# Kernel tuning notes

Hardware: AMD Instinct MI355X
Metric: run time of the kernel (lower is better)

## Reference

```python
import jax, jax.numpy as jnp
import numpy as np

N_NODES = 50000
N_EDGES = 250000
D_IN, D_HID, D_OUT = 768, 256, 2


def _sage_conv(x, src, dst, W_l, b_l, W_r, n_nodes):
    # PyG SAGEConv (aggr='mean', root_weight=True):
    #   out[i] = lin_l(mean_{j in N(i)} x[j]) + lin_r(x[i])
    msg = x[src]  # [E, d] gather of source-node features
    agg = jax.ops.segment_sum(msg, dst, num_segments=n_nodes)
    cnt = jax.ops.segment_sum(jnp.ones((src.shape[0],), x.dtype), dst,
                              num_segments=n_nodes)
    agg = agg / jnp.maximum(cnt, 1.0)[:, None]
    return agg @ W_l.T + b_l + x @ W_r.T


def setup_inputs() -> dict:
    key = jax.random.key(0)
    ks = jax.random.split(key, 7)
    x = jax.random.normal(ks[0], (N_NODES, D_IN), dtype=jnp.float32)
    edge_index = jax.random.randint(ks[1], (2, N_EDGES), 0, N_NODES,
                                    dtype=jnp.int64)
    s1 = 1.0 / np.sqrt(D_IN)
    s2 = 1.0 / np.sqrt(D_HID)
    W1_l = jax.random.uniform(ks[2], (D_HID, D_IN), jnp.float32, -s1, s1)
    W1_r = jax.random.uniform(ks[3], (D_HID, D_IN), jnp.float32, -s1, s1)
    b1 = jnp.zeros((D_HID,), jnp.float32)
    W2_l = jax.random.uniform(ks[4], (D_OUT, D_HID), jnp.float32, -s2, s2)
    W2_r = jax.random.uniform(ks[5], (D_OUT, D_HID), jnp.float32, -s2, s2)
    b2 = jnp.zeros((D_OUT,), jnp.float32)
    return {"x": x, "edge_index": edge_index,
            "W1_l": W1_l, "b1": b1, "W1_r": W1_r,
            "W2_l": W2_l, "b2": b2, "W2_r": W2_r}


def reference(x, edge_index, W1_l, b1, W1_r, W2_l, b2, W2_r):
    src, dst = edge_index[0], edge_index[1]
    n = x.shape[0]
    h = _sage_conv(x, src, dst, W1_l, b1, W1_r, n)
    h = jax.nn.relu(h)
    # dropout is identity in eval mode (deterministic reference)
    out = _sage_conv(h, src, dst, W2_l, b2, W2_r, n)
    return out
```

## Files before the change

kernel.cpp:

```cpp
#include <hip/hip_runtime.h>
#include <stdint.h>


#define D_IN  768
#define D_HID 256
#define N1    512
#define KITERS (D_IN / 32)

typedef __attribute__((ext_vector_type(8))) short short8;
typedef __attribute__((ext_vector_type(4))) float f32x4;

__device__ __forceinline__ void async_copy16(const void* g, void* l) {
  __builtin_amdgcn_global_load_lds(
      (const __attribute__((address_space(1))) unsigned int*)g,
      (__attribute__((address_space(3))) unsigned int*)l,
      16, 0, 0);
}

__device__ __forceinline__ unsigned short f2bf(float f) {
  union { float f; unsigned u; } v; v.f = f;
  unsigned r = v.u + 0x7FFFu + ((v.u >> 16) & 1u);
  return (unsigned short)(r >> 16);
}

__device__ __forceinline__ float bf2f(unsigned short b) {
  union { unsigned u; float f; } v; v.u = ((unsigned)b) << 16;
  return v.f;
}


__global__ void cvtidx_k(const void* __restrict__ eidx,
                         int* __restrict__ src32, int* __restrict__ dst32,
                         int* __restrict__ counts, int E) {
  __shared__ int flag32;
  int tid = threadIdx.x;
  int i = blockIdx.x * 256 + tid;
  unsigned v = (i < E) ? ((const unsigned int*)eidx)[2 * (size_t)i + 1] : 0u;
  unsigned long long any = __ballot(v != 0u);
  if (tid == 0) flag32 = 0;
  __syncthreads();
  if ((tid & 63) == 0 && any) flag32 = 1;
  __syncthreads();
  if (i >= E) return;
  int s, d;
  if (flag32) {
    const int* p = (const int*)eidx;
    s = p[i]; d = p[E + i];
  } else {
    const long long* p = (const long long*)eidx;
    s = (int)p[i]; d = (int)p[E + i];
  }
  src32[i] = s;
  dst32[i] = d;
  atomicAdd(&counts[d], 1);
}

__global__ void scanA_k(const int* __restrict__ counts,
                        int* __restrict__ blockSums, int M) {
  __shared__ int ts[256];
  int b = blockIdx.x, t = threadIdx.x;
  int base = b * 1024 + t * 4;
  int s = 0;
#pragma unroll
  for (int k = 0; k < 4; k++) { int i = base + k; if (i < M) s += counts[i]; }
  ts[t] = s;
  __syncthreads();
  for (int off = 128; off > 0; off >>= 1) {
    if (t < off) ts[t] += ts[t + off];
    __syncthreads();
  }
  if (t == 0) blockSums[b] = ts[0];
}

__global__ void scanC_k(const int* __restrict__ counts,
                        const int* __restrict__ bsums,
                        int* __restrict__ offs, int* __restrict__ cursor,
                        int M, int E, int nb) {
  __shared__ int ts[256];
  __shared__ int bofs;
  int b = blockIdx.x, t = threadIdx.x;
  if (t < 64) {
    int v = (t < nb) ? bsums[t] : 0;
    int orig = v;
#pragma unroll
    for (int off = 1; off < 64; off <<= 1) {
      int u = __shfl_up(v, off);
      if (t >= off) v += u;
    }
    if (t == b) bofs = v - orig;
  }
  int base = b * 1024 + t * 4;
  int v[4]; int s = 0;
#pragma unroll
  for (int k = 0; k < 4; k++) {
    int i = base + k;
    v[k] = (i < M) ? counts[i] : 0;
    s += v[k];
  }
  ts[t] = s;
  __syncthreads();
  for (int off = 1; off < 256; off <<= 1) {
    int x = (t >= off) ? ts[t - off] : 0;
    __syncthreads();
    ts[t] += x;
    __syncthreads();
  }
  int run = bofs + ts[t] - s;
#pragma unroll
  for (int k = 0; k < 4; k++) {
    int i = base + k;
    if (i < M) { offs[i] = run; cursor[i] = run; run += v[k]; }
  }
  if (b == 0 && t == 0) offs[M] = E;
}

__global__ void fill_k(const int* __restrict__ src, const int* __restrict__ dst,
                       int* __restrict__ cursor, int* __restrict__ csr, int E) {
  int i = blockIdx.x * 256 + threadIdx.x;
  if (i >= E) return;
  int pos = atomicAdd(&cursor[dst[i]], 1);
  csr[pos] = src[i];
}


__global__ void cvtw_k(const float* __restrict__ W1l, const float* __restrict__ W1r,
                       unsigned short* __restrict__ wb) {
  int idx = blockIdx.x * 256 + threadIdx.x;
  int total = N1 * (D_IN / 8);
  if (idx >= total) return;
  int row = idx / (D_IN / 8);
  int cpos = (idx % (D_IN / 8)) * 8;
  const float* p = (row < D_HID) ? (W1l + (size_t)row * D_IN + cpos)
                                 : (W1r + (size_t)(row - D_HID) * D_IN + cpos);
  float4 f0 = *(const float4*)p;
  float4 f1 = *(const float4*)(p + 4);
  short8 o;
  o[0] = (short)f2bf(f0.x); o[1] = (short)f2bf(f0.y);
  o[2] = (short)f2bf(f0.z); o[3] = (short)f2bf(f0.w);
  o[4] = (short)f2bf(f1.x); o[5] = (short)f2bf(f1.y);
  o[6] = (short)f2bf(f1.z); o[7] = (short)f2bf(f1.w);
  *(short8*)(wb + (size_t)idx * 8) = o;
}

__global__ void cvtx_k(const float* __restrict__ x,
                       unsigned short* __restrict__ xb, int M, int Mp) {
  int idx = blockIdx.x * 256 + threadIdx.x;
  int total = Mp * (D_IN / 8);
  if (idx >= total) return;
  int row = idx / (D_IN / 8);
  short8 o;
  if (row < M) {
    int col = (idx % (D_IN / 8)) * 8;
    const float* p = x + (size_t)row * D_IN + col;
    float4 f0 = *(const float4*)p;
    float4 f1 = *(const float4*)(p + 4);
    o[0] = (short)f2bf(f0.x); o[1] = (short)f2bf(f0.y);
    o[2] = (short)f2bf(f0.z); o[3] = (short)f2bf(f0.w);
    o[4] = (short)f2bf(f1.x); o[5] = (short)f2bf(f1.y);
    o[6] = (short)f2bf(f1.z); o[7] = (short)f2bf(f1.w);
  } else {
    o = (short8)0;
  }
  *(short8*)(xb + (size_t)idx * 8) = o;
}

__global__ __launch_bounds__(256) void gemm_k(
    const unsigned short* __restrict__ xb,
    const unsigned short* __restrict__ wb,
    unsigned short* __restrict__ Cb, int MT, int mtPerXcd) {
  __shared__ unsigned short As[2][128 * 32];
  __shared__ unsigned short Bs[2][128 * 32];

  const int bid = blockIdx.x;
  const int xcd = bid & 7;
  const int j   = bid >> 3;
  const int mt  = xcd * mtPerXcd + (j >> 2);
  if (mt >= MT) return;
  const int m0 = mt * 128;
  const int n0 = (j & 3) * 128;

  const int tid  = threadIdx.x;
  const int lane = tid & 63;
  const int wid  = tid >> 6;
  const int wr = wid >> 1, wc = wid & 1;
  const int l15  = lane & 15;
  const int quad = lane >> 4;

  const int arow0 = tid >> 2, akg = tid & 3;
  const unsigned short* axp0 = xb + (size_t)(m0 + arow0) * D_IN + akg * 8;
  const unsigned short* axp1 = xb + (size_t)(m0 + arow0 + 64) * D_IN + akg * 8;
  const int aoff0 = tid * 8;
  const int aoff1 = (tid + 256) * 8;

  const int brow = (tid >> 6) * 16 + (tid & 15);
  const int bcg  = (tid >> 4) & 3;
  const unsigned short* bgp0 = wb + (size_t)(n0 + brow) * D_IN + bcg * 8;
  const unsigned short* bgp1 = wb + (size_t)(n0 + brow + 64) * D_IN + bcg * 8;
  const int boff0 = tid * 8;
  const int boff1 = (tid + 256) * 8;

  f32x4 acc[4][4];
#pragma unroll
  for (int r = 0; r < 4; r++)
#pragma unroll
    for (int c = 0; c < 4; c++) acc[r][c] = (f32x4)0.0f;

#define STAGE(P, kk)                                                          \
  {                                                                           \
    const int kn = (kk) * 32;                                                 \
    async_copy16(axp0 + kn, &As[P][aoff0]);                                   \
    async_copy16(axp1 + kn, &As[P][aoff1]);                                   \
    async_copy16(bgp0 + kn, &Bs[P][boff0]);                                   \
    async_copy16(bgp1 + kn, &Bs[P][boff1]);                                   \
  }

#define READ_FRAGS(P, a, b)                                                   \
  _Pragma("unroll")                                                           \
  for (int r = 0; r < 4; r++)                                                 \
    a[r] = *(const short8*)&As[P][(wr * 64 + r * 16 + l15) * 32 + quad * 8];  \
  _Pragma("unroll")                                                           \
  for (int c = 0; c < 4; c++)                                                 \
    b[c] = *(const short8*)&Bs[P][(wc * 4 + c) * 512 + quad * 128 + l15 * 8];

#define MFMA16(a, b)                                                          \
  _Pragma("unroll")                                                           \
  for (int r = 0; r < 4; r++)                                                 \
    _Pragma("unroll")                                                         \
    for (int c = 0; c < 4; c++)                                               \
      acc[r][c] = __builtin_amdgcn_mfma_f32_16x16x32_bf16(a[r], b[c],         \
                                                          acc[r][c], 0, 0, 0);

#define GEMM_BODY(P, kk)                                                      \
  {                                                                           \
    short8 a[4], b[4];                                                        \
    READ_FRAGS(P, a, b)                                                       \
    asm volatile("s_waitcnt lgkmcnt(0)" ::: "memory");                        \
    __builtin_amdgcn_s_barrier();                                             \
    STAGE(P, (kk) + 2)                                                        \
    MFMA16(a, b)                                                              \
    asm volatile("s_waitcnt vmcnt(4)" ::: "memory");                          \
    __builtin_amdgcn_s_barrier();                                             \
  }

  STAGE(0, 0)
  STAGE(1, 1)
  asm volatile("s_waitcnt vmcnt(4)" ::: "memory");
  __builtin_amdgcn_s_barrier();

  for (int it = 0; it < KITERS - 2; it += 2) {
    GEMM_BODY(0, it)
    GEMM_BODY(1, it + 1)
  }

  {
    short8 a[4], b[4];
    READ_FRAGS(0, a, b)
    MFMA16(a, b)
    asm volatile("s_waitcnt vmcnt(0)" ::: "memory");
    __builtin_amdgcn_s_barrier();
  }
  {
    short8 a[4], b[4];
    READ_FRAGS(1, a, b)
    MFMA16(a, b)
  }
#undef GEMM_BODY
#undef MFMA16
#undef READ_FRAGS
#undef STAGE

  const int crow0 = m0 + wr * 64;
  const int ccol0 = n0 + wc * 64;
#pragma unroll
  for (int r = 0; r < 4; r++)
#pragma unroll
    for (int c = 0; c < 4; c++) {
      int col = ccol0 + c * 16 + l15;
#pragma unroll
      for (int reg = 0; reg < 4; reg++) {
        int row = crow0 + r * 16 + quad * 4 + reg;
        Cb[(size_t)row * N1 + col] = f2bf(acc[r][c][reg]);
      }
    }
}

__global__ void agg_l2_k(const unsigned short* __restrict__ Cb,
                         const int* __restrict__ offs, const int* __restrict__ csr,
                         const float* __restrict__ b1,
                         const float* __restrict__ W2l, const float* __restrict__ W2r,
                         float4* __restrict__ rs, int M) {
  int tid = threadIdx.x;
  int lane = tid & 63;
  int wid = tid >> 6;
  int i = blockIdx.x * 4 + wid;
  if (i >= M) return;
  int c = lane * 4;
  float4 bv  = *(const float4*)(b1 + c);
  float4 wl0 = *(const float4*)(W2l + c);
  float4 wl1 = *(const float4*)(W2l + D_HID + c);
  float4 wr0 = *(const float4*)(W2r + c);
  float4 wr1 = *(const float4*)(W2r + D_HID + c);
  int s = offs[i], e = offs[i + 1];
  ushort4 q = *(const ushort4*)(Cb + (size_t)i * N1 + D_HID + c);
  float ax = 0.f, ay = 0.f, az = 0.f, aw = 0.f;
  float bx = 0.f, by = 0.f, bz = 0.f, bw = 0.f;
  int t = s;
  for (; t + 2 <= e; t += 2) {
    int j0 = csr[t];
    int j1 = csr[t + 1];
    ushort4 v0 = *(const ushort4*)(Cb + (size_t)j0 * N1 + c);
    ushort4 v1 = *(const ushort4*)(Cb + (size_t)j1 * N1 + c);
    ax += bf2f(v0.x); ay += bf2f(v0.y); az += bf2f(v0.z); aw += bf2f(v0.w);
    bx += bf2f(v1.x); by += bf2f(v1.y); bz += bf2f(v1.z); bw += bf2f(v1.w);
  }
  if (t < e) {
    int j = csr[t];
    ushort4 v = *(const ushort4*)(Cb + (size_t)j * N1 + c);
    ax += bf2f(v.x); ay += bf2f(v.y); az += bf2f(v.z); aw += bf2f(v.w);
  }
  ax += bx; ay += by; az += bz; aw += bw;
  float inv = 1.0f / fmaxf((float)(e - s), 1.0f);
  float h0 = fmaxf(ax * inv + bv.x + bf2f(q.x), 0.0f);
  float h1 = fmaxf(ay * inv + bv.y + bf2f(q.y), 0.0f);
  float h2 = fmaxf(az * inv + bv.z + bf2f(q.z), 0.0f);
  float h3 = fmaxf(aw * inv + bv.w + bf2f(q.w), 0.0f);
  float r0 = h0 * wl0.x + h1 * wl0.y + h2 * wl0.z + h3 * wl0.w;
  float r1 = h0 * wl1.x + h1 * wl1.y + h2 * wl1.z + h3 * wl1.w;
  float s0 = h0 * wr0.x + h1 * wr0.y + h2 * wr0.z + h3 * wr0.w;
  float s1 = h0 * wr1.x + h1 * wr1.y + h2 * wr1.z + h3 * wr1.w;
#pragma unroll
  for (int off = 32; off > 0; off >>= 1) {
    r0 += __shfl_xor(r0, off);
    r1 += __shfl_xor(r1, off);
    s0 += __shfl_xor(s0, off);
    s1 += __shfl_xor(s1, off);
  }
  if (lane == 0) rs[i] = make_float4(r0, r1, s0, s1);
}

__global__ void final_k(const float4* __restrict__ rs, const int* __restrict__ offs,
                        const int* __restrict__ csr, const float* __restrict__ b2,
                        float* __restrict__ out, int M) {
  int i = blockIdx.x * 256 + threadIdx.x;
  if (i >= M) return;
  int s = offs[i], e = offs[i + 1];
  float a0 = 0.0f, a1 = 0.0f, b0 = 0.0f, b1 = 0.0f;
  int t = s;
  for (; t + 2 <= e; t += 2) {
    float4 v0 = rs[csr[t]];
    float4 v1 = rs[csr[t + 1]];
    a0 += v0.x; a1 += v0.y;
    b0 += v1.x; b1 += v1.y;
  }
  if (t < e) { float4 v = rs[csr[t]]; a0 += v.x; a1 += v.y; }
  a0 += b0; a1 += b1;
  float inv = 1.0f / fmaxf((float)(e - s), 1.0f);
  float4 me = rs[i];
  out[2 * i + 0] = a0 * inv + b2[0] + me.z;
  out[2 * i + 1] = a1 * inv + b2[1] + me.w;
}


extern "C" void kernel_launch(void* const* d_in, const int* in_sizes, int n_in,
                              void* d_out, int out_size, void* d_ws, size_t ws_size,
                              hipStream_t stream) {
  const float* x   = (const float*)d_in[0];
  const void*  eix = d_in[1];
  const float* W1l = (const float*)d_in[2];
  const float* b1  = (const float*)d_in[3];
  const float* W1r = (const float*)d_in[4];
  const float* W2l = (const float*)d_in[5];
  const float* b2  = (const float*)d_in[6];
  const float* W2r = (const float*)d_in[7];
  float* out = (float*)d_out;

  const int M  = in_sizes[0] / D_IN;
  const int E  = in_sizes[1] / 2;
  const int Mp = ((M + 127) / 128) * 128;
  const int nb = (M + 1023) / 1024;
  const int MT = Mp / 128;
  const int mtPerXcd = (MT + 7) / 8;
  const int gemmBlocks = 8 * mtPerXcd * 4;

  char* ws = (char*)d_ws;
  size_t off = 0;
  auto alloc = [&](size_t b) { size_t o = off; off += (b + 255) & ~(size_t)255; return o; };
  size_t oCounts = alloc((size_t)M * 4);
  size_t zeroBytes = (size_t)M * 4;
  size_t oOffs   = alloc((size_t)(M + 1) * 4);
  size_t oCursor = alloc((size_t)M * 4);
  size_t oCsr    = alloc((size_t)E * 4);
  size_t oSrc    = alloc((size_t)E * 4);
  size_t oDst    = alloc((size_t)E * 4);
  size_t oBSums  = alloc(64 * 4);
  size_t oWb     = alloc((size_t)N1 * D_IN * 2);
  size_t oC      = alloc((size_t)Mp * N1 * 2);
  size_t oRs     = alloc((size_t)M * 16);
  size_t oXb     = alloc((size_t)Mp * D_IN * 2);
  (void)ws_size; (void)n_in; (void)out_size;

  int* counts = (int*)(ws + oCounts);
  int* offs   = (int*)(ws + oOffs);
  int* cursor = (int*)(ws + oCursor);
  int* csr    = (int*)(ws + oCsr);
  int* src32  = (int*)(ws + oSrc);
  int* dst32  = (int*)(ws + oDst);
  int* bsums  = (int*)(ws + oBSums);
  unsigned short* wb = (unsigned short*)(ws + oWb);
  unsigned short* Cb = (unsigned short*)(ws + oC);
  float4* rs = (float4*)(ws + oRs);
  unsigned short* xb = (unsigned short*)(ws + oXb);

  hipMemsetAsync(counts, 0, zeroBytes, stream);

  int gE = (E + 255) / 256;
  cvtidx_k<<<gE, 256, 0, stream>>>(eix, src32, dst32, counts, E);
  scanA_k<<<nb, 256, 0, stream>>>(counts, bsums, M);
  scanC_k<<<nb, 256, 0, stream>>>(counts, bsums, offs, cursor, M, E, nb);
  fill_k<<<gE, 256, 0, stream>>>(src32, dst32, cursor, csr, E);

  int gW = (N1 * (D_IN / 8) + 255) / 256;
  cvtw_k<<<gW, 256, 0, stream>>>(W1l, W1r, wb);

  int gX = (Mp * (D_IN / 8) + 255) / 256;
  cvtx_k<<<gX, 256, 0, stream>>>(x, xb, M, Mp);

  gemm_k<<<gemmBlocks, 256, 0, stream>>>(xb, wb, Cb, MT, mtPerXcd);

  agg_l2_k<<<(M + 3) / 4, 256, 0, stream>>>(Cb, offs, csr, b1, W2l, W2r, rs, M);
  final_k<<<(M + 255) / 256, 256, 0, stream>>>(rs, offs, csr, b2, out, M);
}
```

Baseline: 387.0 us.

## Fuse prep kernels, split GEMM output into Cl/Cr, wave-cooperative neighbor gather

Merges the edge-index conversion, weight conversion and x conversion kernels into one launch that dispatches on block index, which removes two launch gaps and lets the three run concurrently. The GEMM now writes the lin_l and lin_r halves into two separate contiguous 256-wide buffers, so gathered neighbor rows are packed more densely and do not share space with the unused root half. The aggregation kernel loads up to 64 CSR indices per wave at once and broadcasts them with shuffles, unrolling four independent gathers to raise memory-level parallelism. The trade-off is extra shuffle work and more registers held per lane.

```diff
diff --git a/kernel.cpp b/kernel.cpp
--- a/kernel.cpp
+++ b/kernel.cpp
@@ -28,31 +28,80 @@
   return v.f;
 }
 
-
-__global__ void cvtidx_k(const void* __restrict__ eidx,
-                         int* __restrict__ src32, int* __restrict__ dst32,
-                         int* __restrict__ counts, int E) {
-  __shared__ int flag32;
-  int tid = threadIdx.x;
-  int i = blockIdx.x * 256 + tid;
-  unsigned v = (i < E) ? ((const unsigned int*)eidx)[2 * (size_t)i + 1] : 0u;
-  unsigned long long any = __ballot(v != 0u);
-  if (tid == 0) flag32 = 0;
-  __syncthreads();
-  if ((tid & 63) == 0 && any) flag32 = 1;
-  __syncthreads();
-  if (i >= E) return;
-  int s, d;
-  if (flag32) {
-    const int* p = (const int*)eidx;
-    s = p[i]; d = p[E + i];
-  } else {
-    const long long* p = (const long long*)eidx;
-    s = (int)p[i]; d = (int)p[E + i];
-  }
-  src32[i] = s;
-  dst32[i] = d;
-  atomicAdd(&counts[d], 1);
+__global__ void prep_k(const void* __restrict__ eidx,
+                       int* __restrict__ src32, int* __restrict__ dst32,
+                       int* __restrict__ counts, int E,
+                       const float* __restrict__ W1l, const float* __restrict__ W1r,
+                       unsigned short* __restrict__ wb,
+                       const float* __restrict__ x,
+                       unsigned short* __restrict__ xb, int M, int Mp,
+                       int gE, int gW) {
+  const int tid = threadIdx.x;
+  const int bid = blockIdx.x;
+
+  if (bid < gE) {
+    __shared__ int flag32;
+    int i = bid * 256 + tid;
+    unsigned v = (i < E) ? ((const unsigned int*)eidx)[2 * (size_t)i + 1] : 0u;
+    unsigned long long any = __ballot(v != 0u);
+    if (tid == 0) flag32 = 0;
+    __syncthreads();
+    if ((tid & 63) == 0 && any) flag32 = 1;
+    __syncthreads();
+    if (i >= E) return;
+    int s, d;
+    if (flag32) {
+      const int* p = (const int*)eidx;
+      s = p[i]; d = p[E + i];
+    } else {
+      const long long* p = (const long long*)eidx;
+      s = (int)p[i]; d = (int)p[E + i];
+    }
+    src32[i] = s;
+    dst32[i] = d;
+    atomicAdd(&counts[d], 1);
+    return;
+  }
+
+  if (bid < gE + gW) {
+    int idx = (bid - gE) * 256 + tid;
+    int total = N1 * (D_IN / 8);
+    if (idx >= total) return;
+    int row = idx / (D_IN / 8);
+    int cpos = (idx % (D_IN / 8)) * 8;
+    const float* p = (row < D_HID) ? (W1l + (size_t)row * D_IN + cpos)
+                                   : (W1r + (size_t)(row - D_HID) * D_IN + cpos);
+    float4 f0 = *(const float4*)p;
+    float4 f1 = *(const float4*)(p + 4);
+    short8 o;
+    o[0] = (short)f2bf(f0.x); o[1] = (short)f2bf(f0.y);
+    o[2] = (short)f2bf(f0.z); o[3] = (short)f2bf(f0.w);
+    o[4] = (short)f2bf(f1.x); o[5] = (short)f2bf(f1.y);
+    o[6] = (short)f2bf(f1.z); o[7] = (short)f2bf(f1.w);
+    *(short8*)(wb + (size_t)idx * 8) = o;
+    return;
+  }
+
+  {
+    int idx = (bid - gE - gW) * 256 + tid;
+    int total = Mp * (D_IN / 8);
+    if (idx >= total) return;
+    int row = idx / (D_IN / 8);
+    short8 o;
+    if (row < M) {
+      int col = (idx % (D_IN / 8)) * 8;
+      const float* p = x + (size_t)row * D_IN + col;
+      float4 f0 = *(const float4*)p;
+      float4 f1 = *(const float4*)(p + 4);
+      o[0] = (short)f2bf(f0.x); o[1] = (short)f2bf(f0.y);
+      o[2] = (short)f2bf(f0.z); o[3] = (short)f2bf(f0.w);
+      o[4] = (short)f2bf(f1.x); o[5] = (short)f2bf(f1.y);
+      o[6] = (short)f2bf(f1.z); o[7] = (short)f2bf(f1.w);
+    } else {
+      o = (short8)0;
+    }
+    *(short8*)(xb + (size_t)idx * 8) = o;
+  }
 }
 
 __global__ void scanA_k(const int* __restrict__ counts,
@@ -122,52 +171,11 @@
   csr[pos] = src[i];
 }
 
-
-__global__ void cvtw_k(const float* __restrict__ W1l, const float* __restrict__ W1r,
-                       unsigned short* __restrict__ wb) {
-  int idx = blockIdx.x * 256 + threadIdx.x;
-  int total = N1 * (D_IN / 8);
-  if (idx >= total) return;
-  int row = idx / (D_IN / 8);
-  int cpos = (idx % (D_IN / 8)) * 8;
-  const float* p = (row < D_HID) ? (W1l + (size_t)row * D_IN + cpos)
-                                 : (W1r + (size_t)(row - D_HID) * D_IN + cpos);
-  float4 f0 = *(const float4*)p;
-  float4 f1 = *(const float4*)(p + 4);
-  short8 o;
-  o[0] = (short)f2bf(f0.x); o[1] = (short)f2bf(f0.y);
-  o[2] = (short)f2bf(f0.z); o[3] = (short)f2bf(f0.w);
-  o[4] = (short)f2bf(f1.x); o[5] = (short)f2bf(f1.y);
-  o[6] = (short)f2bf(f1.z); o[7] = (short)f2bf(f1.w);
-  *(short8*)(wb + (size_t)idx * 8) = o;
-}
-
-__global__ void cvtx_k(const float* __restrict__ x,
-                       unsigned short* __restrict__ xb, int M, int Mp) {
-  int idx = blockIdx.x * 256 + threadIdx.x;
-  int total = Mp * (D_IN / 8);
-  if (idx >= total) return;
-  int row = idx / (D_IN / 8);
-  short8 o;
-  if (row < M) {
-    int col = (idx % (D_IN / 8)) * 8;
-    const float* p = x + (size_t)row * D_IN + col;
-    float4 f0 = *(const float4*)p;
-    float4 f1 = *(const float4*)(p + 4);
-    o[0] = (short)f2bf(f0.x); o[1] = (short)f2bf(f0.y);
-    o[2] = (short)f2bf(f0.z); o[3] = (short)f2bf(f0.w);
-    o[4] = (short)f2bf(f1.x); o[5] = (short)f2bf(f1.y);
-    o[6] = (short)f2bf(f1.z); o[7] = (short)f2bf(f1.w);
-  } else {
-    o = (short8)0;
-  }
-  *(short8*)(xb + (size_t)idx * 8) = o;
-}
-
 __global__ __launch_bounds__(256) void gemm_k(
     const unsigned short* __restrict__ xb,
     const unsigned short* __restrict__ wb,
-    unsigned short* __restrict__ Cb, int MT, int mtPerXcd) {
+    unsigned short* __restrict__ Cl, unsigned short* __restrict__ Cr,
+    int MT, int mtPerXcd) {
   __shared__ unsigned short As[2][128 * 32];
   __shared__ unsigned short Bs[2][128 * 32];
 
@@ -269,8 +277,10 @@
 #undef READ_FRAGS
 #undef STAGE
 
+  unsigned short* dstC = (n0 < 256) ? Cl : Cr;
+  const int ncb = n0 & 255;
   const int crow0 = m0 + wr * 64;
-  const int ccol0 = n0 + wc * 64;
+  const int ccol0 = ncb + wc * 64;
 #pragma unroll
   for (int r = 0; r < 4; r++)
 #pragma unroll
@@ -279,12 +289,13 @@
 #pragma unroll
       for (int reg = 0; reg < 4; reg++) {
         int row = crow0 + r * 16 + quad * 4 + reg;
-        Cb[(size_t)row * N1 + col] = f2bf(acc[r][c][reg]);
+        dstC[(size_t)row * D_HID + col] = f2bf(acc[r][c][reg]);
       }
     }
 }
 
-__global__ void agg_l2_k(const unsigned short* __restrict__ Cb,
+__global__ void agg_l2_k(const unsigned short* __restrict__ Cl,
+                         const unsigned short* __restrict__ Cr,
                          const int* __restrict__ offs, const int* __restrict__ csr,
                          const float* __restrict__ b1,
                          const float* __restrict__ W2l, const float* __restrict__ W2r,
@@ -301,24 +312,40 @@
   float4 wr0 = *(const float4*)(W2r + c);
   float4 wr1 = *(const float4*)(W2r + D_HID + c);
   int s = offs[i], e = offs[i + 1];
-  ushort4 q = *(const ushort4*)(Cb + (size_t)i * N1 + D_HID + c);
-  float ax = 0.f, ay = 0.f, az = 0.f, aw = 0.f;
-  float bx = 0.f, by = 0.f, bz = 0.f, bw = 0.f;
-  int t = s;
-  for (; t + 2 <= e; t += 2) {
-    int j0 = csr[t];
-    int j1 = csr[t + 1];
-    ushort4 v0 = *(const ushort4*)(Cb + (size_t)j0 * N1 + c);
-    ushort4 v1 = *(const ushort4*)(Cb + (size_t)j1 * N1 + c);
-    ax += bf2f(v0.x); ay += bf2f(v0.y); az += bf2f(v0.z); aw += bf2f(v0.w);
-    bx += bf2f(v1.x); by += bf2f(v1.y); bz += bf2f(v1.z); bw += bf2f(v1.w);
-  }
-  if (t < e) {
-    int j = csr[t];
-    ushort4 v = *(const ushort4*)(Cb + (size_t)j * N1 + c);
-    ax += bf2f(v.x); ay += bf2f(v.y); az += bf2f(v.z); aw += bf2f(v.w);
-  }
-  ax += bx; ay += by; az += bz; aw += bw;
+  ushort4 q = *(const ushort4*)(Cr + (size_t)i * D_HID + c);
+  float a0x = 0.f, a0y = 0.f, a0z = 0.f, a0w = 0.f;
+  float a1x = 0.f, a1y = 0.f, a1z = 0.f, a1w = 0.f;
+  float a2x = 0.f, a2y = 0.f, a2z = 0.f, a2w = 0.f;
+  float a3x = 0.f, a3y = 0.f, a3z = 0.f, a3w = 0.f;
+  for (int base = s; base < e; base += 64) {
+    int rem = e - base;
+    int m = rem < 64 ? rem : 64;
+    int jj = csr[base + (lane < m ? lane : m - 1)];
+    int t = 0;
+    for (; t + 4 <= m; t += 4) {
+      int j0 = __shfl(jj, t);
+      int j1 = __shfl(jj, t + 1);
+      int j2 = __shfl(jj, t + 2);
+      int j3 = __shfl(jj, t + 3);
+      ushort4 v0 = *(const ushort4*)(Cl + (size_t)j0 * D_HID + c);
+      ushort4 v1 = *(const ushort4*)(Cl + (size_t)j1 * D_HID + c);
+      ushort4 v2 = *(const ushort4*)(Cl + (size_t)j2 * D_HID + c);
+      ushort4 v3 = *(const ushort4*)(Cl + (size_t)j3 * D_HID + c);
+      a0x += bf2f(v0.x); a0y += bf2f(v0.y); a0z += bf2f(v0.z); a0w += bf2f(v0.w);
+      a1x += bf2f(v1.x); a1y += bf2f(v1.y); a1z += bf2f(v1.z); a1w += bf2f(v1.w);
+      a2x += bf2f(v2.x); a2y += bf2f(v2.y); a2z += bf2f(v2.z); a2w += bf2f(v2.w);
+      a3x += bf2f(v3.x); a3y += bf2f(v3.y); a3z += bf2f(v3.z); a3w += bf2f(v3.w);
+    }
+    for (; t < m; t++) {
+      int j0 = __shfl(jj, t);
+      ushort4 v = *(const ushort4*)(Cl + (size_t)j0 * D_HID + c);
+      a0x += bf2f(v.x); a0y += bf2f(v.y); a0z += bf2f(v.z); a0w += bf2f(v.w);
+    }
+  }
+  float ax = (a0x + a1x) + (a2x + a3x);
+  float ay = (a0y + a1y) + (a2y + a3y);
+  float az = (a0z + a1z) + (a2z + a3z);
+  float aw = (a0w + a1w) + (a2w + a3w);
   float inv = 1.0f / fmaxf((float)(e - s), 1.0f);
   float h0 = fmaxf(ax * inv + bv.x + bf2f(q.x), 0.0f);
   float h1 = fmaxf(ay * inv + bv.y + bf2f(q.y), 0.0f);
@@ -394,7 +421,8 @@
   size_t oDst    = alloc((size_t)E * 4);
   size_t oBSums  = alloc(64 * 4);
   size_t oWb     = alloc((size_t)N1 * D_IN * 2);
-  size_t oC      = alloc((size_t)Mp * N1 * 2);
+  size_t oCl     = alloc((size_t)Mp * D_HID * 2);
+  size_t oCr     = alloc((size_t)Mp * D_HID * 2);
   size_t oRs     = alloc((size_t)M * 16);
   size_t oXb     = alloc((size_t)Mp * D_IN * 2);
   (void)ws_size; (void)n_in; (void)out_size;
@@ -407,26 +435,25 @@
   int* dst32  = (int*)(ws + oDst);
   int* bsums  = (int*)(ws + oBSums);
   unsigned short* wb = (unsigned short*)(ws + oWb);
-  unsigned short* Cb = (unsigned short*)(ws + oC);
+  unsigned short* Cl = (unsigned short*)(ws + oCl);
+  unsigned short* Cr = (unsigned short*)(ws + oCr);
   float4* rs = (float4*)(ws + oRs);
   unsigned short* xb = (unsigned short*)(ws + oXb);
 
   hipMemsetAsync(counts, 0, zeroBytes, stream);
 
   int gE = (E + 255) / 256;
-  cvtidx_k<<<gE, 256, 0, stream>>>(eix, src32, dst32, counts, E);
+  int gW = (N1 * (D_IN / 8) + 255) / 256;
+  int gX = (Mp * (D_IN / 8) + 255) / 256;
+  prep_k<<<gE + gW + gX, 256, 0, stream>>>(eix, src32, dst32, counts, E,
+                                           W1l, W1r, wb, x, xb, M, Mp, gE, gW);
   scanA_k<<<nb, 256, 0, stream>>>(counts, bsums, M);
   scanC_k<<<nb, 256, 0, stream>>>(counts, bsums, offs, cursor, M, E, nb);
-  fill_k<<<gE, 256, 0, stream>>>(src32, dst32, cursor, csr, E);
-
-  int gW = (N1 * (D_IN / 8) + 255) / 256;
-  cvtw_k<<<gW, 256, 0, stream>>>(W1l, W1r, wb);
-
-  int gX = (Mp * (D_IN / 8) + 255) / 256;
-  cvtx_k<<<gX, 256, 0, stream>>>(x, xb, M, Mp);
-
-  gemm_k<<<gemmBlocks, 256, 0, stream>>>(xb, wb, Cb, MT, mtPerXcd);
-
-  agg_l2_k<<<(M + 3) / 4, 256, 0, stream>>>(Cb, offs, csr, b1, W2l, W2r, rs, M);
+  fill_k<<<(E + 255) / 256, 256, 0, stream>>>(src32, dst32, cursor, csr, E);
+
+  gemm_k<<<gemmBlocks, 256, 0, stream>>>(xb, wb, Cl, Cr, MT, mtPerXcd);
+
+  agg_l2_k<<<(M + 3) / 4, 256, 0, stream>>>(Cl, Cr, offs, csr, b1, W2l, W2r,
+                                            rs, M);
   final_k<<<(M + 255) / 256, 256, 0, stream>>>(rs, offs, csr, b2, out, M);
 }
```

After: 376.2 us. -2.8%, faster.
